# Kernel optimization log

Hardware: AMD Instinct MI355X
Metric: run time of the kernel (lower is better)

Reference implementation:

```python
import jax, jax.numpy as jnp
import numpy as np

SCALE = 32.0  # hardcoded self.scale in the module


def fwht(x):
    """Fast Walsh-Hadamard transform along last dim (power-of-2 length).
    Equivalent to x @ H_n (Sylvester Hadamard), unnormalized."""
    orig_shape = x.shape
    n = orig_shape[-1]
    x = x.reshape(-1, n)
    h = 2
    while h <= n:
        x = x.reshape(-1, n // h, h)
        half = h // 2
        a = x[:, :, :half]
        b = x[:, :, half:]
        x = jnp.concatenate([a + b, a - b], axis=-1)
        h *= 2
    return x.reshape(orig_shape)


def setup_inputs() -> dict:
    key = jax.random.key(0)
    k1, k2, k3, k4, k5 = jax.random.split(key, 5)
    B, S, N, M = 8, 2048, 4096, 4096
    x = jax.random.normal(k1, (B, S, N), dtype=jnp.float32)
    W = jax.random.normal(k2, (M, N), dtype=jnp.float32) * 0.02  # nn.Linear weight [out, in]
    SU = jax.random.uniform(k3, (N,), dtype=jnp.float32, minval=0.5, maxval=1.5)
    SV = jax.random.uniform(k4, (M,), dtype=jnp.float32, minval=0.5, maxval=1.5)
    Wscale = jax.random.uniform(k5, (M,), dtype=jnp.float32, minval=0.5, maxval=1.5)
    return {"x": x, "W": W, "SU": SU, "SV": SV, "Wscale": Wscale}


def reference(x, W, SU, SV, Wscale):
    n = SU.shape[0]
    m = SV.shape[0]
    inv_sqrt_n = 1.0 / np.sqrt(n).astype(np.float32)
    inv_sqrt_m = 1.0 / np.sqrt(m).astype(np.float32)
    h = x.reshape(-1, n) * SU                       # per-channel input scale
    h = fwht(h) * (inv_sqrt_n / SCALE)              # normalized Hadamard rotation / scale
    h = jnp.einsum('tn,mn->tm', h, W) * Wscale      # linear + per-channel weight scale
    h = fwht(h) * inv_sqrt_m                        # inverse (normalized) Hadamard rotation
    h = h * (SV * SCALE)                            # per-channel output scale * scale
    return h.reshape(*x.shape[:-1], m)
```

## Files before the change

kernel.cpp:

```cpp
#include <hip/hip_runtime.h>
#include <hip/hip_bf16.h>

typedef __bf16 bf16x8 __attribute__((ext_vector_type(8)));
typedef float f32x4 __attribute__((ext_vector_type(4)));

__device__ __forceinline__ void gload16(const void* g, void* l) {
  __builtin_amdgcn_global_load_lds(
      (const __attribute__((address_space(1))) void*)g,
      (__attribute__((address_space(3))) void*)l, 16, 0, 0);
}

__device__ __forceinline__ unsigned short f2bf(float f) {
  __hip_bfloat16 h = __float2bfloat16(f);
  union { __hip_bfloat16 h; unsigned short u; } c;
  c.h = h;
  return c.u;
}

__device__ __forceinline__ void fwht16(float v[16]) {
#pragma unroll
  for (int s = 1; s < 16; s <<= 1) {
#pragma unroll
    for (int i = 0; i < 16; i++) {
      if ((i & s) == 0) {
        float a = v[i], b = v[i | s];
        v[i] = a + b;
        v[i | s] = a - b;
      }
    }
  }
}

__global__ __launch_bounds__(256) void fwht1_kernel(
    const float* __restrict__ x, const float* __restrict__ SU,
    unsigned short* __restrict__ H1) {
  __shared__ float lds[256 * 17];
  const int t = threadIdx.x;
  const size_t row = blockIdx.x;
  const float* xr = x + row * 4096;
  float v[16];
#pragma unroll
  for (int n2 = 0; n2 < 16; n2++) {
    int n = n2 * 256 + t;
    v[n2] = xr[n] * SU[n];
  }
  fwht16(v);
  const int n1 = t >> 4, n0 = t & 15;
#pragma unroll
  for (int j2 = 0; j2 < 16; j2++) lds[(j2 * 16 + n1) * 17 + n0] = v[j2];
  __syncthreads();
#pragma unroll
  for (int k = 0; k < 16; k++) v[k] = lds[((t >> 4) * 16 + k) * 17 + (t & 15)];
  fwht16(v);
#pragma unroll
  for (int k = 0; k < 16; k++) lds[((t >> 4) * 16 + k) * 17 + (t & 15)] = v[k];
  __syncthreads();
#pragma unroll
  for (int k = 0; k < 16; k++) v[k] = lds[t * 17 + k];
  fwht16(v);
  const float cst = 1.0f / 2048.0f;
  union { unsigned short u[16]; uint4 q[2]; } o;
#pragma unroll
  for (int k = 0; k < 16; k++) o.u[k] = f2bf(v[k] * cst);
  uint4* dst = (uint4*)(H1 + row * 4096 + (size_t)t * 16);
  dst[0] = o.q[0];
  dst[1] = o.q[1];
}

__global__ __launch_bounds__(256) void convw_kernel(
    const float4* __restrict__ W4, const float* __restrict__ Wscale,
    uint2* __restrict__ Wb4, int total4, int Nq) {
  int i = blockIdx.x * 256 + threadIdx.x;
  if (i >= total4) return;
  float4 w = W4[i];
  float s = Wscale[i / Nq];
  unsigned int lo = (unsigned)f2bf(w.x * s) | ((unsigned)f2bf(w.y * s) << 16);
  unsigned int hi = (unsigned)f2bf(w.z * s) | ((unsigned)f2bf(w.w * s) << 16);
  Wb4[i] = make_uint2(lo, hi);
}


#define BAR() __builtin_amdgcn_s_barrier()
#define SCHED() __builtin_amdgcn_sched_barrier(0)
#define GATE2()                              \
  do {                                       \
    SCHED();                                 \
    asm volatile("s_waitcnt vmcnt(2)");      \
    SCHED();                                 \
  } while (0)
#define GATE0()                              \
  do {                                       \
    SCHED();                                 \
    asm volatile("s_waitcnt vmcnt(0)");      \
    SCHED();                                 \
  } while (0)
#define LGKM0() asm volatile("s_waitcnt lgkmcnt(0)")
#define LGKM8() asm volatile("s_waitcnt lgkmcnt(8)")

__device__ __forceinline__ void stage_half(const unsigned short* __restrict__ g,
                                           unsigned short* l, int tid, int K) {
#pragma unroll
  for (int i = 0; i < 2; i++) {
    int idx = i * 512 + tid;
    int r = idx >> 3;
    int c = (idx & 7) ^ (r & 7);
    gload16(g + (size_t)r * K + c * 8, l + idx * 8);
  }
}

#define STAGE_A(d, hh, kt) \
  stage_half(Abase + (size_t)(hh)*128 * K + (size_t)(kt)*64, &As[d][(hh)*8192], tid, K)
#define STAGE_B(d, hh, kt) \
  stage_half(Bbase + (size_t)(hh)*128 * K + (size_t)(kt)*64, &Bs[d][(hh)*8192], tid, K)

#define LOAD_A(d, m)                                                          \
  {                                                                           \
    _Pragma("unroll") for (int i = 0; i < 4; i++) {                           \
      _Pragma("unroll") for (int ks = 0; ks < 2; ks++) {                      \
        int r = wm * 128 + (m)*64 + i * 16 + fr;                              \
        int kc = ks * 4 + lhi;                                                \
        ah[i][ks] = *(const bf16x8*)&As[d][r * 64 + ((kc ^ (r & 7)) << 3)];   \
      }                                                                       \
    }                                                                         \
  }

#define LOAD_B(d, v, dst)                                                     \
  {                                                                           \
    _Pragma("unroll") for (int j = 0; j < 2; j++) {                           \
      _Pragma("unroll") for (int ks = 0; ks < 2; ks++) {                      \
        int r = wn * 64 + (v)*32 + j * 16 + fr;                               \
        int kc = ks * 4 + lhi;                                                \
        dst[j][ks] = *(const bf16x8*)&Bs[d][r * 64 + ((kc ^ (r & 7)) << 3)];  \
      }                                                                       \
    }                                                                         \
  }

#define MFMA_PH(m, v, bvx)                                                    \
  {                                                                           \
    __builtin_amdgcn_s_setprio(1);                                            \
    _Pragma("unroll") for (int i = 0; i < 4; i++)                             \
      _Pragma("unroll") for (int j = 0; j < 2; j++)                           \
        _Pragma("unroll") for (int ks = 0; ks < 2; ks++)                      \
          acc[(m)*4 + i][(v)*2 + j] = __builtin_amdgcn_mfma_f32_16x16x32_bf16( \
              ah[i][ks], bvx[j][ks], acc[(m)*4 + i][(v)*2 + j], 0, 0, 0);     \
    __builtin_amdgcn_s_setprio(0);                                            \
  }

__global__ __launch_bounds__(512, 2) void gemm8_kernel(
    const unsigned short* __restrict__ A, const unsigned short* __restrict__ B,
    float* __restrict__ C, int M, int K, int NT) {
  __shared__ __align__(16) unsigned short As[2][256 * 64];
  __shared__ __align__(16) unsigned short Bs[2][256 * 64];
  const int nbn = M >> 8;
  const int cpx = gridDim.x >> 3;
  int bid = blockIdx.x;
  bid = (bid & 7) * cpx + (bid >> 3);
  const int brow = (bid / nbn) << 8;
  const int bcol = (bid % nbn) << 8;
  const int tid = threadIdx.x;
  const int lane = tid & 63;
  const int w = tid >> 6;
  const int wm = w >> 2;
  const int wn = w & 3;
  const int fr = lane & 15;
  const int lhi = lane >> 4;

  const unsigned short* Abase = A + (size_t)brow * K;
  const unsigned short* Bbase = B + (size_t)bcol * K;

  f32x4 acc[8][4];
#pragma unroll
  for (int i = 0; i < 8; i++)
#pragma unroll
    for (int j = 0; j < 4; j++) acc[i][j] = (f32x4){0.f, 0.f, 0.f, 0.f};
  bf16x8 ah[4][2], bv0[2][2], bv1[2][2];

  STAGE_A(0, 0, 0);
  STAGE_A(0, 1, 0);
  STAGE_B(0, 0, 0);
  STAGE_B(0, 1, 0);
  STAGE_A(1, 0, 1);
  GATE2();
  BAR();

  const int NTT = NT / 2;
#pragma unroll 1
  for (int t = 0; t < NTT; ++t) {
    const bool last = (t == NTT - 1);
    const int u1 = 2 * t + 1, u2 = 2 * t + 2, u3 = 2 * t + 3;
    LOAD_A(0, 0);
    LOAD_B(0, 0, bv0);
    STAGE_A(1, 1, u1);
    LGKM8();
    BAR();
    LGKM0();
    MFMA_PH(0, 0, bv0);
    BAR();
    LOAD_B(0, 1, bv1);
    STAGE_B(1, 0, u1);
    BAR();
    LGKM0();
    MFMA_PH(0, 1, bv1);
    BAR();
    LOAD_A(0, 1);
    STAGE_B(1, 1, u1);
    BAR();
    LGKM0();
    MFMA_PH(1, 1, bv1);
    BAR();
    if (!last) {
      STAGE_A(0, 0, u2);
      GATE2();
    } else {
      GATE0();
    }
    BAR();
    MFMA_PH(1, 0, bv0);
    BAR();
    LOAD_A(1, 0);
    LOAD_B(1, 0, bv0);
    if (!last) STAGE_A(0, 1, u2);
    LGKM8();
    BAR();
    LGKM0();
    MFMA_PH(0, 0, bv0);
    BAR();
    LOAD_B(1, 1, bv1);
    if (!last) STAGE_B(0, 0, u2);
    BAR();
    LGKM0();
    MFMA_PH(0, 1, bv1);
    BAR();
    LOAD_A(1, 1);
    if (!last) STAGE_B(0, 1, u2);
    BAR();
    LGKM0();
    MFMA_PH(1, 1, bv1);
    BAR();
    if (!last) {
      STAGE_A(1, 0, u3);
      GATE2();
    }
    BAR();
    MFMA_PH(1, 0, bv0);
    BAR();
  }

  const int crow0 = brow + wm * 128 + lhi * 4;
  const int ccol0 = bcol + wn * 64 + fr;
#pragma unroll
  for (int mi = 0; mi < 8; mi++)
#pragma unroll
    for (int nj = 0; nj < 4; nj++)
#pragma unroll
      for (int q = 0; q < 4; q++)
        C[(size_t)(crow0 + mi * 16 + q) * M + ccol0 + nj * 16] = acc[mi][nj][q];
}

__global__ __launch_bounds__(256) void fwht2_kernel(
    float* __restrict__ Y, const float* __restrict__ SV) {
  __shared__ float lds[256 * 17];
  const int t = threadIdx.x;
  const size_t row = blockIdx.x;
  float* yr = Y + row * 4096;
  float v[16];
#pragma unroll
  for (int n2 = 0; n2 < 16; n2++) v[n2] = yr[n2 * 256 + t];
  fwht16(v);
  const int n1 = t >> 4, n0 = t & 15;
#pragma unroll
  for (int j2 = 0; j2 < 16; j2++) lds[(j2 * 16 + n1) * 17 + n0] = v[j2];
  __syncthreads();
#pragma unroll
  for (int k = 0; k < 16; k++) v[k] = lds[((t >> 4) * 16 + k) * 17 + (t & 15)];
  fwht16(v);
#pragma unroll
  for (int k = 0; k < 16; k++) lds[((t >> 4) * 16 + k) * 17 + (t & 15)] = v[k];
  __syncthreads();
#pragma unroll
  for (int k = 0; k < 16; k++) v[k] = lds[t * 17 + k];
  fwht16(v);
  float outv[16];
#pragma unroll
  for (int k = 0; k < 16; k++) outv[k] = v[k] * 0.5f * SV[(size_t)t * 16 + k];
  float4* dst = (float4*)(yr + (size_t)t * 16);
#pragma unroll
  for (int k = 0; k < 4; k++)
    dst[k] = make_float4(outv[4 * k], outv[4 * k + 1], outv[4 * k + 2],
                         outv[4 * k + 3]);
}

extern "C" void kernel_launch(void* const* d_in, const int* in_sizes, int n_in,
                              void* d_out, int out_size, void* d_ws,
                              size_t ws_size, hipStream_t stream) {
  const float* x = (const float*)d_in[0];
  const float* W = (const float*)d_in[1];
  const float* SU = (const float*)d_in[2];
  const float* SV = (const float*)d_in[3];
  const float* Wscale = (const float*)d_in[4];
  const int N = in_sizes[2];
  const int M = in_sizes[3];
  const int T = in_sizes[0] / N;

  unsigned short* H1 = (unsigned short*)d_ws;
  unsigned short* Wb = H1 + (size_t)T * N;
  float* out = (float*)d_out;

  fwht1_kernel<<<T, 256, 0, stream>>>(x, SU, H1);
  const int total4 = (int)(((long)M * N) / 4);
  convw_kernel<<<(total4 + 255) / 256, 256, 0, stream>>>(
      (const float4*)W, Wscale, (uint2*)Wb, total4, N / 4);
  const int NT = N / 64;
  gemm8_kernel<<<(T / 256) * (M / 256), 512, 0, stream>>>(H1, Wb, out, M, N, NT);
  fwht2_kernel<<<T, 256, 0, stream>>>(out, SV);
}
```

Measured before the change: 758.9 us.

## Restructure GEMM main loop into 8-phase schedule with B-first staging and interleaved A halves

Reorders the double-buffered GEMM main loop so B tiles are staged first and the two A halves are stored interleaved by wave row, letting each MFMA phase consume a half that was just loaded. Removes the explicit lgkmcnt waits between LDS reads and MFMAs, replacing them with finer vmcnt gates (6/4) placed after MFMA phases. Register B fragments ping-pong between two buffers across phases, and B is preloaded before the loop. The aim is more overlap of global-to-LDS loads and LDS reads with MFMA work. Dropping the lgkmcnt waits relies on the compiler inserting the needed waits for the LDS reads, and the wait counts must match the new staging order.

```diff
diff --git a/kernel.cpp b/kernel.cpp
--- a/kernel.cpp
+++ b/kernel.cpp
@@ -82,6 +82,18 @@
 
 #define BAR() __builtin_amdgcn_s_barrier()
 #define SCHED() __builtin_amdgcn_sched_barrier(0)
+#define GATE6()                              \
+  do {                                       \
+    SCHED();                                 \
+    asm volatile("s_waitcnt vmcnt(6)");      \
+    SCHED();                                 \
+  } while (0)
+#define GATE4()                              \
+  do {                                       \
+    SCHED();                                 \
+    asm volatile("s_waitcnt vmcnt(4)");      \
+    SCHED();                                 \
+  } while (0)
 #define GATE2()                              \
   do {                                       \
     SCHED();                                 \
@@ -94,34 +106,44 @@
     asm volatile("s_waitcnt vmcnt(0)");      \
     SCHED();                                 \
   } while (0)
-#define LGKM0() asm volatile("s_waitcnt lgkmcnt(0)")
-#define LGKM8() asm volatile("s_waitcnt lgkmcnt(8)")
-
-__device__ __forceinline__ void stage_half(const unsigned short* __restrict__ g,
-                                           unsigned short* l, int tid, int K) {
+
+__device__ __forceinline__ void stage_A(const unsigned short* __restrict__ Ab,
+                                        unsigned short* lr, int h, int kt,
+                                        int tid, int K) {
 #pragma unroll
   for (int i = 0; i < 2; i++) {
     int idx = i * 512 + tid;
-    int r = idx >> 3;
-    int c = (idx & 7) ^ (r & 7);
-    gload16(g + (size_t)r * K + c * 8, l + idx * 8);
-  }
-}
-
-#define STAGE_A(d, hh, kt) \
-  stage_half(Abase + (size_t)(hh)*128 * K + (size_t)(kt)*64, &As[d][(hh)*8192], tid, K)
+    int rl = idx >> 3;
+    int c = (idx & 7) ^ (rl & 7);
+    int grow = (rl >> 6) * 128 + h * 64 + (rl & 63);
+    gload16(Ab + (size_t)grow * K + (size_t)kt * 64 + c * 8, lr + idx * 8);
+  }
+}
+__device__ __forceinline__ void stage_B(const unsigned short* __restrict__ Bb,
+                                        unsigned short* lr, int tid, int K) {
+#pragma unroll
+  for (int i = 0; i < 2; i++) {
+    int idx = i * 512 + tid;
+    int rl = idx >> 3;
+    int c = (idx & 7) ^ (rl & 7);
+    gload16(Bb + (size_t)rl * K + c * 8, lr + idx * 8);
+  }
+}
+
+#define STAGE_A(d, h, kt) stage_A(Abase, &As[d][(h)*8192], (h), (kt), tid, K)
 #define STAGE_B(d, hh, kt) \
-  stage_half(Bbase + (size_t)(hh)*128 * K + (size_t)(kt)*64, &Bs[d][(hh)*8192], tid, K)
-
-#define LOAD_A(d, m)                                                          \
-  {                                                                           \
-    _Pragma("unroll") for (int i = 0; i < 4; i++) {                           \
-      _Pragma("unroll") for (int ks = 0; ks < 2; ks++) {                      \
-        int r = wm * 128 + (m)*64 + i * 16 + fr;                              \
-        int kc = ks * 4 + lhi;                                                \
-        ah[i][ks] = *(const bf16x8*)&As[d][r * 64 + ((kc ^ (r & 7)) << 3)];   \
-      }                                                                       \
-    }                                                                         \
+  stage_B(Bbase + (size_t)(hh)*128 * K + (size_t)(kt)*64, &Bs[d][(hh)*8192], tid, K)
+
+#define LOAD_A(d, m)                                                           \
+  {                                                                            \
+    _Pragma("unroll") for (int i = 0; i < 4; i++) {                            \
+      _Pragma("unroll") for (int ks = 0; ks < 2; ks++) {                       \
+        int rl = wm * 64 + i * 16 + fr;                                        \
+        int kc = ks * 4 + lhi;                                                 \
+        ah[i][ks] =                                                            \
+            *(const bf16x8*)&As[d][(m)*8192 + rl * 64 + ((kc ^ (rl & 7)) << 3)]; \
+      }                                                                        \
+    }                                                                          \
   }
 
 #define LOAD_B(d, v, dst)                                                     \
@@ -173,15 +195,16 @@
   for (int i = 0; i < 8; i++)
 #pragma unroll
     for (int j = 0; j < 4; j++) acc[i][j] = (f32x4){0.f, 0.f, 0.f, 0.f};
-  bf16x8 ah[4][2], bv0[2][2], bv1[2][2];
-
+  bf16x8 ah[4][2], bvP[2][2], bvQ[2][2];
+
+  STAGE_B(0, 0, 0);
+  STAGE_B(0, 1, 0);
   STAGE_A(0, 0, 0);
   STAGE_A(0, 1, 0);
-  STAGE_B(0, 0, 0);
-  STAGE_B(0, 1, 0);
-  STAGE_A(1, 0, 1);
+  STAGE_B(1, 0, 1);
   GATE2();
   BAR();
+  LOAD_B(0, 0, bvP);
 
   const int NTT = NT / 2;
 #pragma unroll 1
@@ -189,60 +212,50 @@
     const bool last = (t == NTT - 1);
     const int u1 = 2 * t + 1, u2 = 2 * t + 2, u3 = 2 * t + 3;
     LOAD_A(0, 0);
-    LOAD_B(0, 0, bv0);
+    STAGE_B(1, 1, u1);
+    BAR();
+    MFMA_PH(0, 0, bvP);
+    BAR();
+    LOAD_B(0, 1, bvQ);
+    STAGE_A(1, 0, u1);
+    BAR();
+    MFMA_PH(0, 1, bvQ);
+    GATE6();
+    BAR();
+    LOAD_A(0, 1);
     STAGE_A(1, 1, u1);
-    LGKM8();
-    BAR();
-    LGKM0();
-    MFMA_PH(0, 0, bv0);
-    BAR();
-    LOAD_B(0, 1, bv1);
-    STAGE_B(1, 0, u1);
-    BAR();
-    LGKM0();
-    MFMA_PH(0, 1, bv1);
-    BAR();
-    LOAD_A(0, 1);
-    STAGE_B(1, 1, u1);
-    BAR();
-    LGKM0();
-    MFMA_PH(1, 1, bv1);
-    BAR();
-    if (!last) {
-      STAGE_A(0, 0, u2);
-      GATE2();
-    } else {
-      GATE0();
-    }
-    BAR();
-    MFMA_PH(1, 0, bv0);
+    BAR();
+    MFMA_PH(1, 1, bvQ);
+    GATE4();
+    BAR();
+    LOAD_B(1, 0, bvQ);
+    if (!last) STAGE_B(0, 0, u2);
+    BAR();
+    MFMA_PH(1, 0, bvP);
+    if (!last) { GATE4(); } else { GATE0(); }
     BAR();
     LOAD_A(1, 0);
-    LOAD_B(1, 0, bv0);
+    if (!last) STAGE_B(0, 1, u2);
+    BAR();
+    MFMA_PH(0, 0, bvQ);
+    BAR();
+    LOAD_B(1, 1, bvP);
+    if (!last) STAGE_A(0, 0, u2);
+    BAR();
+    MFMA_PH(0, 1, bvP);
+    if (!last) GATE6();
+    BAR();
+    LOAD_A(1, 1);
     if (!last) STAGE_A(0, 1, u2);
-    LGKM8();
-    BAR();
-    LGKM0();
-    MFMA_PH(0, 0, bv0);
-    BAR();
-    LOAD_B(1, 1, bv1);
-    if (!last) STAGE_B(0, 0, u2);
-    BAR();
-    LGKM0();
-    MFMA_PH(0, 1, bv1);
-    BAR();
-    LOAD_A(1, 1);
-    if (!last) STAGE_B(0, 1, u2);
-    BAR();
-    LGKM0();
-    MFMA_PH(1, 1, bv1);
-    BAR();
-    if (!last) {
-      STAGE_A(1, 0, u3);
-      GATE2();
-    }
-    BAR();
-    MFMA_PH(1, 0, bv0);
+    BAR();
+    MFMA_PH(1, 1, bvP);
+    if (!last) GATE4();
+    BAR();
+    LOAD_B(0, 0, bvP);
+    if (!last) STAGE_B(1, 0, u3);
+    BAR();
+    MFMA_PH(1, 0, bvQ);
+    if (!last) GATE4();
     BAR();
   }
 
```

New measurement: 823.0 us. 1.08x slower.

## Restructure GEMM main loop barriers to halve sync points and overlap staging

Applied to the files above, without the earlier changes.

Cuts the ping-pong GEMM loop from two barriers per MFMA phase to one. It drops the explicit lgkmcnt waits so the compiler can place LDS waits itself, and issues global-to-LDS staging before the fragment reads. The vmcnt gate now sits after the last MFMA phase of each half. The MFMA loop order is also changed so ks is the outer loop, which interleaves independent accumulators. The aim is to reduce barrier stalls and let MFMA overlap more with memory traffic, at the risk of LDS read/write hazards if the single barriers do not fully order staging writes against fragment reads.

```diff
diff --git a/kernel.cpp b/kernel.cpp
--- a/kernel.cpp
+++ b/kernel.cpp
@@ -94,8 +94,6 @@
     asm volatile("s_waitcnt vmcnt(0)");      \
     SCHED();                                 \
   } while (0)
-#define LGKM0() asm volatile("s_waitcnt lgkmcnt(0)")
-#define LGKM8() asm volatile("s_waitcnt lgkmcnt(8)")
 
 __device__ __forceinline__ void stage_half(const unsigned short* __restrict__ g,
                                            unsigned short* l, int tid, int K) {
@@ -138,9 +136,9 @@
 #define MFMA_PH(m, v, bvx)                                                    \
   {                                                                           \
     __builtin_amdgcn_s_setprio(1);                                            \
-    _Pragma("unroll") for (int i = 0; i < 4; i++)                             \
-      _Pragma("unroll") for (int j = 0; j < 2; j++)                           \
-        _Pragma("unroll") for (int ks = 0; ks < 2; ks++)                      \
+    _Pragma("unroll") for (int ks = 0; ks < 2; ks++)                          \
+      _Pragma("unroll") for (int i = 0; i < 4; i++)                           \
+        _Pragma("unroll") for (int j = 0; j < 2; j++)                         \
           acc[(m)*4 + i][(v)*2 + j] = __builtin_amdgcn_mfma_f32_16x16x32_bf16( \
               ah[i][ks], bvx[j][ks], acc[(m)*4 + i][(v)*2 + j], 0, 0, 0);     \
     __builtin_amdgcn_s_setprio(0);                                            \
@@ -181,69 +179,46 @@
   STAGE_B(0, 1, 0);
   STAGE_A(1, 0, 1);
   GATE2();
-  BAR();
 
   const int NTT = NT / 2;
 #pragma unroll 1
   for (int t = 0; t < NTT; ++t) {
     const bool last = (t == NTT - 1);
     const int u1 = 2 * t + 1, u2 = 2 * t + 2, u3 = 2 * t + 3;
+    BAR();
+    STAGE_A(1, 1, u1);
     LOAD_A(0, 0);
     LOAD_B(0, 0, bv0);
-    STAGE_A(1, 1, u1);
-    LGKM8();
-    BAR();
-    LGKM0();
     MFMA_PH(0, 0, bv0);
     BAR();
+    STAGE_B(1, 0, u1);
     LOAD_B(0, 1, bv1);
-    STAGE_B(1, 0, u1);
-    BAR();
-    LGKM0();
     MFMA_PH(0, 1, bv1);
     BAR();
+    STAGE_B(1, 1, u1);
     LOAD_A(0, 1);
-    STAGE_B(1, 1, u1);
-    BAR();
-    LGKM0();
     MFMA_PH(1, 1, bv1);
     BAR();
-    if (!last) {
-      STAGE_A(0, 0, u2);
-      GATE2();
-    } else {
-      GATE0();
-    }
-    BAR();
+    if (!last) STAGE_A(0, 0, u2);
     MFMA_PH(1, 0, bv0);
-    BAR();
+    if (!last) { GATE2(); } else { GATE0(); }
+    BAR();
+    if (!last) STAGE_A(0, 1, u2);
     LOAD_A(1, 0);
     LOAD_B(1, 0, bv0);
-    if (!last) STAGE_A(0, 1, u2);
-    LGKM8();
-    BAR();
-    LGKM0();
     MFMA_PH(0, 0, bv0);
     BAR();
+    if (!last) STAGE_B(0, 0, u2);
     LOAD_B(1, 1, bv1);
-    if (!last) STAGE_B(0, 0, u2);
-    BAR();
-    LGKM0();
     MFMA_PH(0, 1, bv1);
     BAR();
+    if (!last) STAGE_B(0, 1, u2);
     LOAD_A(1, 1);
-    if (!last) STAGE_B(0, 1, u2);
-    BAR();
-    LGKM0();
     MFMA_PH(1, 1, bv1);
     BAR();
-    if (!last) {
-      STAGE_A(1, 0, u3);
-      GATE2();
-    }
-    BAR();
+    if (!last) STAGE_A(1, 0, u3);
     MFMA_PH(1, 0, bv0);
-    BAR();
+    if (!last) GATE2();
   }
 
   const int crow0 = brow + wm * 128 + lhi * 4;
```

Result: slower. 809.2 us (+6.6%).
